# Kernel tuning notes

Hardware: AMD Instinct MI355X
Metric: run time of the kernel (lower is better)

Reference implementation:

```python
import jax, jax.numpy as jnp
import numpy as np

M, K, N = 8192, 4096, 12288


def setup_inputs() -> dict:
    key = jax.random.key(0)
    k1, k2, k3, k4 = jax.random.split(key, 4)
    input_tensor = jax.random.normal(k1, (1, M, K), dtype=jnp.float32)
    # int8 quantized weight [N, K] and per-output-channel scale [N, 1]
    weight = jax.random.randint(k2, (N, K), -127, 128, dtype=jnp.int32).astype(jnp.int8)
    weight_scale = (jax.random.uniform(k3, (N, 1), dtype=jnp.float32) * 0.01 + 1e-4)
    bias = jax.random.normal(k4, (N,), dtype=jnp.float32) * 0.1
    return {"input_tensor": input_tensor, "weight": weight,
            "weight_scale": weight_scale, "bias": bias}


def reference(input_tensor, weight, weight_scale, bias):
    x = input_tensor[0]  # squeeze(0) -> [M, K]
    # dynamic per-token symmetric int8 quantization: scale = absmax/127
    a_scale = jnp.max(jnp.abs(x), axis=-1, keepdims=True) / 127.0  # [M, 1]
    q = jnp.clip(jnp.round(x / a_scale), -128.0, 127.0)  # int8 values held in f32
    # int8 GEMM accumulated (emulated in f32), then dequant with per-token x per-channel scales
    acc = jnp.einsum('mk,nk->mn', q, weight.astype(jnp.float32))  # [M, N]
    out = acc * a_scale * weight_scale[:, 0][None, :] + bias[None, :]
    return out[None].astype(input_tensor.dtype)  # unsqueeze(0) -> [1, M, N]
```

## Files before the change

### kernel.cpp

```cpp
#include <hip/hip_runtime.h>
#include <cstdint>

#define M_DIM 8192
#define K_DIM 4096
#define N_DIM 12288
#define KTILES (K_DIM / 64)

using i32x4 = __attribute__((ext_vector_type(4))) int;

__device__ inline void gload_lds16(const void* g, void* l) {
    __builtin_amdgcn_global_load_lds(
        (const __attribute__((address_space(1))) void*)g,
        (__attribute__((address_space(3))) void*)l,
        16, 0, 0);
}

__global__ __launch_bounds__(256) void quant_pack(const float* __restrict__ x,
                                                  const int* __restrict__ w32,
                                                  int8_t* __restrict__ qa,
                                                  float* __restrict__ ascale,
                                                  int8_t* __restrict__ wq) {
    const int t = threadIdx.x;
    if (blockIdx.x < M_DIM) {
        const int row = blockIdx.x;
        const float4* xr = (const float4*)(x + (size_t)row * K_DIM);
        float4 v[4];
        float amax = 0.0f;
#pragma unroll
        for (int c = 0; c < 4; ++c) {
            v[c] = xr[t + 256 * c];
            amax = fmaxf(amax, fmaxf(fmaxf(fabsf(v[c].x), fabsf(v[c].y)),
                                     fmaxf(fabsf(v[c].z), fabsf(v[c].w))));
        }
#pragma unroll
        for (int off = 32; off > 0; off >>= 1)
            amax = fmaxf(amax, __shfl_xor(amax, off));
        __shared__ float smax[4];
        if ((t & 63) == 0) smax[t >> 6] = amax;
        __syncthreads();
        amax = fmaxf(fmaxf(smax[0], smax[1]), fmaxf(smax[2], smax[3]));
        const float sc = amax * (1.0f / 127.0f);
        const float inv = (amax > 0.0f) ? (127.0f / amax) : 0.0f;
        if (t == 0) ascale[row] = sc;

        int* q32 = (int*)(qa + (size_t)row * K_DIM);
#pragma unroll
        for (int c = 0; c < 4; ++c) {
            int q0 = (int)rintf(v[c].x * inv);
            int q1 = (int)rintf(v[c].y * inv);
            int q2 = (int)rintf(v[c].z * inv);
            int q3 = (int)rintf(v[c].w * inv);
            q0 = min(127, max(-128, q0));
            q1 = min(127, max(-128, q1));
            q2 = min(127, max(-128, q2));
            q3 = min(127, max(-128, q3));
            q32[t + 256 * c] = (q0 & 255) | ((q1 & 255) << 8) | ((q2 & 255) << 16) | (q3 << 24);
        }
    } else {
        const int pb = blockIdx.x - M_DIM;
        const size_t total4 = (size_t)N_DIM * K_DIM / 4;
        const size_t stride = (size_t)2048 * 256;
        int* out32 = (int*)wq;
        for (size_t i = (size_t)pb * 256 + t; i < total4; i += stride) {
            const int4 v = ((const int4*)w32)[i];
            out32[i] = (v.x & 255) | ((v.y & 255) << 8) | ((v.z & 255) << 16) | (v.w << 24);
        }
    }
}

__global__ __launch_bounds__(512, 2) void gemm_i8(const int8_t* __restrict__ qa,
                                                  const int8_t* __restrict__ wq,
                                                  const float* __restrict__ ascale,
                                                  const float* __restrict__ wscale,
                                                  const float* __restrict__ bias,
                                                  float* __restrict__ out) {
    __shared__ int8_t lds[4][2][256 * 64];

    const int t = threadIdx.x;
    const int lane = t & 63;
    const int wave = t >> 6;
    const int wm = wave >> 2;
    const int wn = wave & 3;
    const int lrow = lane & 15;
    const int lk = lane >> 4;
    const int elr = ((lrow ^ (lrow >> 2)) & 3);

    const int flat = blockIdx.x;
    const int sw = (flat & 7) * 192 + (flat >> 3);
    const int bm = sw / 48;
    const int bn = sw % 48;

    const int rA0 = t >> 2;
    const int rA1 = (t >> 2) + 128;
    const int kA0 = (t & 3) ^ ((rA0 ^ (rA0 >> 2)) & 3);
    const int kA1 = (t & 3) ^ ((rA1 ^ (rA1 >> 2)) & 3);
    const size_t aoff0 = (size_t)(bm * 256 + rA0) * K_DIM + (size_t)kA0 * 16;
    const size_t aoff1 = (size_t)(bm * 256 + rA1) * K_DIM + (size_t)kA1 * 16;
    const size_t boff0 = (size_t)(bn * 256 + rA0) * K_DIM + (size_t)kA0 * 16;
    const size_t boff1 = (size_t)(bn * 256 + rA1) * K_DIM + (size_t)kA1 * 16;

    i32x4 acc[8][4] = {};

#pragma unroll
    for (int p = 0; p < 2; ++p) {
        const size_t ko = (size_t)p * 64;
        gload_lds16(qa + aoff0 + ko, &lds[p][0][t * 16]);
        gload_lds16(qa + aoff1 + ko, &lds[p][0][t * 16 + 8192]);
        gload_lds16(wq + boff0 + ko, &lds[p][1][t * 16]);
        gload_lds16(wq + boff1 + ko, &lds[p][1][t * 16 + 8192]);
    }

    for (int j = 0; j < KTILES; ++j) {
        const int cb = j & 3;
        if (j + 2 < KTILES) {
            const int sb = (j + 2) & 3;
            const size_t ko = (size_t)(j + 2) * 64;
            gload_lds16(qa + aoff0 + ko, &lds[sb][0][t * 16]);
            gload_lds16(qa + aoff1 + ko, &lds[sb][0][t * 16 + 8192]);
            gload_lds16(wq + boff0 + ko, &lds[sb][1][t * 16]);
            gload_lds16(wq + boff1 + ko, &lds[sb][1][t * 16 + 8192]);
            asm volatile("s_waitcnt vmcnt(8)" ::: "memory");
        } else if (j + 1 < KTILES) {
            asm volatile("s_waitcnt vmcnt(4)" ::: "memory");
        } else {
            asm volatile("s_waitcnt vmcnt(0)" ::: "memory");
        }
        __builtin_amdgcn_s_barrier();
        __builtin_amdgcn_sched_barrier(0);

        const int8_t* __restrict__ LA = lds[cb][0];
        const int8_t* __restrict__ LB = lds[cb][1];
        i32x4 af[8], bf[4];
#pragma unroll
        for (int m = 0; m < 8; ++m) {
            const int r = wm * 128 + m * 16 + lrow;
            af[m] = *(const i32x4*)&LA[r * 64 + ((lk ^ elr) << 4)];
        }
#pragma unroll
        for (int n = 0; n < 4; ++n) {
            const int r = wn * 64 + n * 16 + lrow;
            bf[n] = *(const i32x4*)&LB[r * 64 + ((lk ^ elr) << 4)];
        }
        __builtin_amdgcn_s_setprio(1);
#pragma unroll
        for (int m = 0; m < 8; ++m)
#pragma unroll
            for (int n = 0; n < 4; ++n)
                acc[m][n] = __builtin_amdgcn_mfma_i32_16x16x64_i8(af[m], bf[n],
                                                                  acc[m][n], 0, 0, 0);
        __builtin_amdgcn_s_setprio(0);
    }

    const int r0 = bm * 256 + wm * 128;
    const int c0 = bn * 256 + wn * 64;
    float asc[8][4];
#pragma unroll
    for (int m = 0; m < 8; ++m)
#pragma unroll
        for (int j = 0; j < 4; ++j)
            asc[m][j] = ascale[r0 + m * 16 + lk * 4 + j];
#pragma unroll
    for (int n = 0; n < 4; ++n) {
        const int col = c0 + n * 16 + lrow;
        const float wsc = wscale[col];
        const float bb = bias[col];
#pragma unroll
        for (int m = 0; m < 8; ++m) {
#pragma unroll
            for (int j = 0; j < 4; ++j) {
                const int row = r0 + m * 16 + lk * 4 + j;
                out[(size_t)row * N_DIM + col] = (float)acc[m][n][j] * asc[m][j] * wsc + bb;
            }
        }
    }
}

extern "C" void kernel_launch(void* const* d_in, const int* in_sizes, int n_in,
                              void* d_out, int out_size, void* d_ws, size_t ws_size,
                              hipStream_t stream) {
    const float* x = (const float*)d_in[0];
    const int* w32 = (const int*)d_in[1];
    const float* wscale = (const float*)d_in[2];
    const float* bias = (const float*)d_in[3];
    float* out = (float*)d_out;

    int8_t* qa = (int8_t*)d_ws;
    float* ascale = (float*)((char*)d_ws + (size_t)M_DIM * K_DIM);
    int8_t* wq = (int8_t*)((char*)d_ws + (size_t)M_DIM * K_DIM +
                           (size_t)M_DIM * sizeof(float));

    quant_pack<<<M_DIM + 2048, 256, 0, stream>>>(x, w32, qa, ascale, wq);
    gemm_i8<<<1536, 512, 0, stream>>>(qa, wq, ascale, wscale, bias, out);
}
```

Measured before the change: 543.4 us.

## Switch int8 GEMM to 32x32x32 MFMA tiles with a matching LDS swizzle

Replaces the 16x16x64 int8 MFMA with the 32x32x32 variant. Each wave now computes 4x2 fragments of 32x32 over two k-substeps per 64-wide K tile, where before it computed 8x4 fragments of 16x16. The LDS swizzle, fragment loads and epilogue row mapping are rewritten to fit the new layout. The aim is fewer LDS fragment reads per MFMA and fewer instruction issues. The trade-off is a different LDS bank-conflict pattern and a more complex epilogue indexing.

New measurement: 564.3 us. +3.9%, slower.

```diff
diff --git a/kernel.cpp b/kernel.cpp
--- a/kernel.cpp
+++ b/kernel.cpp
@@ -4,9 +4,10 @@
 #define M_DIM 8192
 #define K_DIM 4096
 #define N_DIM 12288
-#define KTILES (K_DIM / 64)
+#define KTILES 64
 
 using i32x4 = __attribute__((ext_vector_type(4))) int;
+using i32x16 = __attribute__((ext_vector_type(16))) int;
 
 __device__ inline void gload_lds16(const void* g, void* l) {
     __builtin_amdgcn_global_load_lds(
@@ -81,25 +82,23 @@
     const int wave = t >> 6;
     const int wm = wave >> 2;
     const int wn = wave & 3;
-    const int lrow = lane & 15;
-    const int lk = lane >> 4;
-    const int elr = ((lrow ^ (lrow >> 2)) & 3);
+    const int l31 = lane & 31;
+    const int lhi = lane >> 5;
+    const int fr = (l31 >> 1) & 3;
 
     const int flat = blockIdx.x;
     const int sw = (flat & 7) * 192 + (flat >> 3);
     const int bm = sw / 48;
     const int bn = sw % 48;
 
-    const int rA0 = t >> 2;
-    const int rA1 = (t >> 2) + 128;
-    const int kA0 = (t & 3) ^ ((rA0 ^ (rA0 >> 2)) & 3);
-    const int kA1 = (t & 3) ^ ((rA1 ^ (rA1 >> 2)) & 3);
-    const size_t aoff0 = (size_t)(bm * 256 + rA0) * K_DIM + (size_t)kA0 * 16;
-    const size_t aoff1 = (size_t)(bm * 256 + rA1) * K_DIM + (size_t)kA1 * 16;
-    const size_t boff0 = (size_t)(bn * 256 + rA0) * K_DIM + (size_t)kA0 * 16;
-    const size_t boff1 = (size_t)(bn * 256 + rA1) * K_DIM + (size_t)kA1 * 16;
-
-    i32x4 acc[8][4] = {};
+    const int row0 = t >> 2;
+    const int g = (t & 3) ^ ((t >> 3) & 3);
+    const size_t aoff0 = (size_t)(bm * 256 + row0) * K_DIM + (size_t)g * 16;
+    const size_t aoff1 = aoff0 + (size_t)128 * K_DIM;
+    const size_t boff0 = (size_t)(bn * 256 + row0) * K_DIM + (size_t)g * 16;
+    const size_t boff1 = boff0 + (size_t)128 * K_DIM;
+
+    i32x16 acc[4][2] = {};
 
 #pragma unroll
     for (int p = 0; p < 2; ++p) {
@@ -130,46 +129,54 @@
 
         const int8_t* __restrict__ LA = lds[cb][0];
         const int8_t* __restrict__ LB = lds[cb][1];
-        i32x4 af[8], bf[4];
-#pragma unroll
-        for (int m = 0; m < 8; ++m) {
-            const int r = wm * 128 + m * 16 + lrow;
-            af[m] = *(const i32x4*)&LA[r * 64 + ((lk ^ elr) << 4)];
-        }
-#pragma unroll
-        for (int n = 0; n < 4; ++n) {
-            const int r = wn * 64 + n * 16 + lrow;
-            bf[n] = *(const i32x4*)&LB[r * 64 + ((lk ^ elr) << 4)];
+        i32x4 af[2][4], bf[2][2];
+#pragma unroll
+        for (int ks = 0; ks < 2; ++ks) {
+#pragma unroll
+            for (int mf = 0; mf < 4; ++mf) {
+                const int r = wm * 128 + mf * 32 + l31;
+                const int slot = (ks * 2 + lhi) ^ fr;
+                af[ks][mf] = *(const i32x4*)&LA[r * 64 + (slot << 4)];
+            }
+#pragma unroll
+            for (int nf = 0; nf < 2; ++nf) {
+                const int r = wn * 64 + nf * 32 + l31;
+                const int slot = (ks * 2 + lhi) ^ fr;
+                bf[ks][nf] = *(const i32x4*)&LB[r * 64 + (slot << 4)];
+            }
         }
         __builtin_amdgcn_s_setprio(1);
 #pragma unroll
-        for (int m = 0; m < 8; ++m)
-#pragma unroll
-            for (int n = 0; n < 4; ++n)
-                acc[m][n] = __builtin_amdgcn_mfma_i32_16x16x64_i8(af[m], bf[n],
-                                                                  acc[m][n], 0, 0, 0);
+        for (int ks = 0; ks < 2; ++ks)
+#pragma unroll
+            for (int mf = 0; mf < 4; ++mf)
+#pragma unroll
+                for (int nf = 0; nf < 2; ++nf)
+                    acc[mf][nf] = __builtin_amdgcn_mfma_i32_32x32x32_i8(
+                        af[ks][mf], bf[ks][nf], acc[mf][nf], 0, 0, 0);
         __builtin_amdgcn_s_setprio(0);
     }
 
     const int r0 = bm * 256 + wm * 128;
     const int c0 = bn * 256 + wn * 64;
-    float asc[8][4];
-#pragma unroll
-    for (int m = 0; m < 8; ++m)
-#pragma unroll
-        for (int j = 0; j < 4; ++j)
-            asc[m][j] = ascale[r0 + m * 16 + lk * 4 + j];
-#pragma unroll
-    for (int n = 0; n < 4; ++n) {
-        const int col = c0 + n * 16 + lrow;
-        const float wsc = wscale[col];
-        const float bb = bias[col];
-#pragma unroll
-        for (int m = 0; m < 8; ++m) {
-#pragma unroll
-            for (int j = 0; j < 4; ++j) {
-                const int row = r0 + m * 16 + lk * 4 + j;
-                out[(size_t)row * N_DIM + col] = (float)acc[m][n][j] * asc[m][j] * wsc + bb;
+#pragma unroll
+    for (int mf = 0; mf < 4; ++mf) {
+        float a16[16];
+#pragma unroll
+        for (int reg = 0; reg < 16; ++reg) {
+            const int rif = (reg & 3) + 8 * (reg >> 2) + 4 * lhi;
+            a16[reg] = ascale[r0 + mf * 32 + rif];
+        }
+#pragma unroll
+        for (int nf = 0; nf < 2; ++nf) {
+            const int col = c0 + nf * 32 + l31;
+            const float wsc = wscale[col];
+            const float bb = bias[col];
+#pragma unroll
+            for (int reg = 0; reg < 16; ++reg) {
+                const int rif = (reg & 3) + 8 * (reg >> 2) + 4 * lhi;
+                const int row = r0 + mf * 32 + rif;
+                out[(size_t)row * N_DIM + col] = (float)acc[mf][nf][reg] * a16[reg] * wsc + bb;
             }
         }
     }
```

## Deepen GEMM prefetch to three stages and split K-tile compute into two phases

Applied to the files above, without the earlier changes.

The prefetch depth rises from two to three tiles in flight across the four LDS buffers. A and B loads are staggered: A is issued at the start of the iteration and B between two half-tile MFMA phases. A fragments are read in two halves to reduce register pressure, and the LDS XOR swizzle changes to a simpler pattern. Each iteration now has extra barriers, and the new swizzle could alter LDS bank conflicts.

New measurement: 555.3 us. 1.02x slower.

```diff
diff --git a/kernel.cpp b/kernel.cpp
--- a/kernel.cpp
+++ b/kernel.cpp
@@ -4,7 +4,7 @@
 #define M_DIM 8192
 #define K_DIM 4096
 #define N_DIM 12288
-#define KTILES (K_DIM / 64)
+#define KT 64
 
 using i32x4 = __attribute__((ext_vector_type(4))) int;
 
@@ -74,7 +74,7 @@
                                                   const float* __restrict__ wscale,
                                                   const float* __restrict__ bias,
                                                   float* __restrict__ out) {
-    __shared__ int8_t lds[4][2][256 * 64];
+    __shared__ int8_t lds[4][2][16384];
 
     const int t = threadIdx.x;
     const int lane = t & 63;
@@ -83,44 +83,50 @@
     const int wn = wave & 3;
     const int lrow = lane & 15;
     const int lk = lane >> 4;
-    const int elr = ((lrow ^ (lrow >> 2)) & 3);
+    const int rslot = (lk ^ ((lrow >> 1) & 3)) << 4;
 
     const int flat = blockIdx.x;
     const int sw = (flat & 7) * 192 + (flat >> 3);
     const int bm = sw / 48;
     const int bn = sw % 48;
 
-    const int rA0 = t >> 2;
-    const int rA1 = (t >> 2) + 128;
-    const int kA0 = (t & 3) ^ ((rA0 ^ (rA0 >> 2)) & 3);
-    const int kA1 = (t & 3) ^ ((rA1 ^ (rA1 >> 2)) & 3);
-    const size_t aoff0 = (size_t)(bm * 256 + rA0) * K_DIM + (size_t)kA0 * 16;
-    const size_t aoff1 = (size_t)(bm * 256 + rA1) * K_DIM + (size_t)kA1 * 16;
-    const size_t boff0 = (size_t)(bn * 256 + rA0) * K_DIM + (size_t)kA0 * 16;
-    const size_t boff1 = (size_t)(bn * 256 + rA1) * K_DIM + (size_t)kA1 * 16;
+    const int g = (t & 3) ^ ((t >> 3) & 3);
+    const size_t aoff0 = (size_t)(bm * 256 + (t >> 2)) * K_DIM + (size_t)g * 16;
+    const size_t aoff1 = aoff0 + (size_t)128 * K_DIM;
+    const size_t boff0 = (size_t)(bn * 256 + (t >> 2)) * K_DIM + (size_t)g * 16;
+    const size_t boff1 = boff0 + (size_t)128 * K_DIM;
+
+#define STAGE_A(sb, jt)                                                      \
+    {                                                                        \
+        gload_lds16(qa + aoff0 + (size_t)(jt) * 64, &lds[sb][0][t * 16]);    \
+        gload_lds16(qa + aoff1 + (size_t)(jt) * 64,                          \
+                    &lds[sb][0][t * 16 + 8192]);                             \
+    }
+#define STAGE_B(sb, jt)                                                      \
+    {                                                                        \
+        gload_lds16(wq + boff0 + (size_t)(jt) * 64, &lds[sb][1][t * 16]);    \
+        gload_lds16(wq + boff1 + (size_t)(jt) * 64,                          \
+                    &lds[sb][1][t * 16 + 8192]);                             \
+    }
 
     i32x4 acc[8][4] = {};
 
 #pragma unroll
-    for (int p = 0; p < 2; ++p) {
-        const size_t ko = (size_t)p * 64;
-        gload_lds16(qa + aoff0 + ko, &lds[p][0][t * 16]);
-        gload_lds16(qa + aoff1 + ko, &lds[p][0][t * 16 + 8192]);
-        gload_lds16(wq + boff0 + ko, &lds[p][1][t * 16]);
-        gload_lds16(wq + boff1 + ko, &lds[p][1][t * 16 + 8192]);
-    }
-
-    for (int j = 0; j < KTILES; ++j) {
+    for (int p = 0; p < 3; ++p) {
+        STAGE_A(p, p);
+        STAGE_B(p, p);
+    }
+
+    for (int j = 0; j < KT; ++j) {
         const int cb = j & 3;
-        if (j + 2 < KTILES) {
-            const int sb = (j + 2) & 3;
-            const size_t ko = (size_t)(j + 2) * 64;
-            gload_lds16(qa + aoff0 + ko, &lds[sb][0][t * 16]);
-            gload_lds16(qa + aoff1 + ko, &lds[sb][0][t * 16 + 8192]);
-            gload_lds16(wq + boff0 + ko, &lds[sb][1][t * 16]);
-            gload_lds16(wq + boff1 + ko, &lds[sb][1][t * 16 + 8192]);
+        const int pb = (j + 3) & 3;
+
+        if (j + 3 < KT) {
+            STAGE_A(pb, j + 3);
+            asm volatile("s_waitcnt vmcnt(10)" ::: "memory");
+        } else if (j + 2 < KT) {
             asm volatile("s_waitcnt vmcnt(8)" ::: "memory");
-        } else if (j + 1 < KTILES) {
+        } else if (j + 1 < KT) {
             asm volatile("s_waitcnt vmcnt(4)" ::: "memory");
         } else {
             asm volatile("s_waitcnt vmcnt(0)" ::: "memory");
@@ -130,25 +136,41 @@
 
         const int8_t* __restrict__ LA = lds[cb][0];
         const int8_t* __restrict__ LB = lds[cb][1];
-        i32x4 af[8], bf[4];
-#pragma unroll
-        for (int m = 0; m < 8; ++m) {
-            const int r = wm * 128 + m * 16 + lrow;
-            af[m] = *(const i32x4*)&LA[r * 64 + ((lk ^ elr) << 4)];
-        }
-#pragma unroll
-        for (int n = 0; n < 4; ++n) {
-            const int r = wn * 64 + n * 16 + lrow;
-            bf[n] = *(const i32x4*)&LB[r * 64 + ((lk ^ elr) << 4)];
-        }
+        i32x4 af[4], bf[4], ah[4];
+#pragma unroll
+        for (int nf = 0; nf < 4; ++nf)
+            bf[nf] = *(const i32x4*)&LB[(wn * 64 + nf * 16 + lrow) * 64 + rslot];
+#pragma unroll
+        for (int mf = 0; mf < 4; ++mf)
+            af[mf] = *(const i32x4*)&LA[(wm * 128 + mf * 16 + lrow) * 64 + rslot];
+        asm volatile("s_waitcnt lgkmcnt(0)" ::: "memory");
+        __builtin_amdgcn_sched_barrier(0);
         __builtin_amdgcn_s_setprio(1);
 #pragma unroll
-        for (int m = 0; m < 8; ++m)
-#pragma unroll
-            for (int n = 0; n < 4; ++n)
-                acc[m][n] = __builtin_amdgcn_mfma_i32_16x16x64_i8(af[m], bf[n],
-                                                                  acc[m][n], 0, 0, 0);
+        for (int mf = 0; mf < 4; ++mf)
+#pragma unroll
+            for (int nf = 0; nf < 4; ++nf)
+                acc[mf][nf] = __builtin_amdgcn_mfma_i32_16x16x64_i8(
+                    af[mf], bf[nf], acc[mf][nf], 0, 0, 0);
         __builtin_amdgcn_s_setprio(0);
+        __builtin_amdgcn_s_barrier();
+
+#pragma unroll
+        for (int mf = 0; mf < 4; ++mf)
+            ah[mf] = *(const i32x4*)&LA[(wm * 128 + (mf + 4) * 16 + lrow) * 64 + rslot];
+        if (j + 3 < KT) STAGE_B(pb, j + 3);
+        __builtin_amdgcn_s_barrier();
+        asm volatile("s_waitcnt lgkmcnt(0)" ::: "memory");
+        __builtin_amdgcn_sched_barrier(0);
+        __builtin_amdgcn_s_setprio(1);
+#pragma unroll
+        for (int mf = 0; mf < 4; ++mf)
+#pragma unroll
+            for (int nf = 0; nf < 4; ++nf)
+                acc[mf + 4][nf] = __builtin_amdgcn_mfma_i32_16x16x64_i8(
+                    ah[mf], bf[nf], acc[mf + 4][nf], 0, 0, 0);
+        __builtin_amdgcn_s_setprio(0);
+        __builtin_amdgcn_s_barrier();
     }
 
     const int r0 = bm * 256 + wm * 128;
@@ -157,8 +179,8 @@
 #pragma unroll
     for (int m = 0; m < 8; ++m)
 #pragma unroll
-        for (int j = 0; j < 4; ++j)
-            asc[m][j] = ascale[r0 + m * 16 + lk * 4 + j];
+        for (int jj = 0; jj < 4; ++jj)
+            asc[m][jj] = ascale[r0 + m * 16 + lk * 4 + jj];
 #pragma unroll
     for (int n = 0; n < 4; ++n) {
         const int col = c0 + n * 16 + lrow;
@@ -167,9 +189,9 @@
 #pragma unroll
         for (int m = 0; m < 8; ++m) {
 #pragma unroll
-            for (int j = 0; j < 4; ++j) {
-                const int row = r0 + m * 16 + lk * 4 + j;
-                out[(size_t)row * N_DIM + col] = (float)acc[m][n][j] * asc[m][j] * wsc + bb;
+            for (int jj = 0; jj < 4; ++jj) {
+                const int row = r0 + m * 16 + lk * 4 + jj;
+                out[(size_t)row * N_DIM + col] = (float)acc[m][n][jj] * asc[m][jj] * wsc + bb;
             }
         }
     }
```
